# Kernel optimization log

Measured on AMD Instinct MI355X. Metric: run time of the kernel, lower is better.

Reference implementation:

```python
import jax, jax.numpy as jnp
import numpy as np

H, KV, Dh = 16, 4, 128
ROPE_BASE = 10000.0


def _rope(x, pos):
    # x: (B, nh, T, Dh); pos: (T,)
    inv = 1.0 / (ROPE_BASE ** (jnp.arange(0, Dh, 2, dtype=jnp.float32) / Dh))  # (Dh/2,)
    freqs = pos.astype(jnp.float32)[:, None] * inv[None, :]                    # (T, Dh/2)
    cos = jnp.cos(freqs).astype(x.dtype)[None, None]                           # (1,1,T,Dh/2)
    sin = jnp.sin(freqs).astype(x.dtype)[None, None]
    x1, x2 = x[..., ::2], x[..., 1::2]
    o1 = x1 * cos - x2 * sin
    o2 = x1 * sin + x2 * cos
    return jnp.stack([o1, o2], axis=-1).reshape(x.shape)


def setup_inputs() -> dict:
    key = jax.random.key(0)
    ks = jax.random.split(key, 5)
    B, T, d = 2, 2048, 2048
    s = 1.0 / np.sqrt(d)
    return {
        "x": jax.random.normal(ks[0], (B, T, d), dtype=jnp.float32),
        "Wq": jax.random.normal(ks[1], (d, H * Dh), dtype=jnp.float32) * s,
        "Wk": jax.random.normal(ks[2], (d, KV * Dh), dtype=jnp.float32) * s,
        "Wv": jax.random.normal(ks[3], (d, KV * Dh), dtype=jnp.float32) * s,
        "Wo": jax.random.normal(ks[4], (H * Dh, d), dtype=jnp.float32) * s,
    }


def reference(x, Wq, Wk, Wv, Wo):
    B, T, d = x.shape
    rep = H // KV
    q = (x @ Wq).reshape(B, T, H, Dh).transpose(0, 2, 1, 3)   # (B,H,T,Dh)
    k = (x @ Wk).reshape(B, T, KV, Dh).transpose(0, 2, 1, 3)  # (B,KV,T,Dh)
    v = (x @ Wv).reshape(B, T, KV, Dh).transpose(0, 2, 1, 3)

    pos = jnp.arange(T)
    q = _rope(q, pos)
    k = _rope(k, pos)

    # GQA repeat_kv: (B,KV,T,Dh) -> (B,H,T,Dh), heads repeated consecutively
    k_full = jnp.repeat(k, rep, axis=1)
    v_full = jnp.repeat(v, rep, axis=1)

    scale = 1.0 / np.sqrt(Dh)
    scores = jnp.einsum('bhqd,bhkd->bhqk', q, k_full) * scale  # (B,H,T,T)
    causal = jnp.tril(jnp.ones((T, T), dtype=bool))
    scores = jnp.where(causal[None, None], scores, -jnp.inf)
    attn = jax.nn.softmax(scores, axis=-1)
    out = jnp.einsum('bhqk,bhkd->bhqd', attn, v_full)          # (B,H,T,Dh)
    out = out.transpose(0, 2, 1, 3).reshape(B, T, H * Dh)
    return out @ Wo
```

## Files before the change

kernel.cpp:

```cpp
#include <hip/hip_runtime.h>
#include <stdint.h>

typedef __bf16 bf16;
typedef __bf16 bf16x8 __attribute__((ext_vector_type(8)));
typedef __bf16 bf16x4 __attribute__((ext_vector_type(4)));
typedef float  f32x4  __attribute__((ext_vector_type(4)));

#define T_SEQ  2048
#define NHEAD  16
#define DHEAD  128
#define DMODEL 2048
#define NQKV   3072
#define UNROLL _Pragma("unroll")

__device__ __forceinline__ void gload_lds16(const void* g, void* l) {
  __builtin_amdgcn_global_load_lds(
      (const __attribute__((address_space(1))) uint32_t*)g,
      (__attribute__((address_space(3))) uint32_t*)l, 16, 0, 0);
}

__device__ __forceinline__ void twt_body(const float* __restrict__ W,
                                         bf16* __restrict__ WT, int K, int N,
                                         int bx, int by, float (*t)[65]) {
  int k0 = bx * 64, n0 = by * 64;
  int r4 = threadIdx.x >> 6, c = threadIdx.x & 63;
#pragma unroll
  for (int i = 0; i < 16; i++) {
    int r = i * 4 + r4;
    t[r][c] = W[(size_t)(k0 + r) * N + n0 + c];
  }
  __syncthreads();
#pragma unroll
  for (int i = 0; i < 16; i++) {
    int r = i * 4 + r4;
    WT[(size_t)(n0 + r) * K + k0 + c] = (bf16)t[c][r];
  }
}

__global__ __launch_bounds__(256) void k_prep(const float* __restrict__ x,
                                              const float* __restrict__ Wq,
                                              const float* __restrict__ Wk,
                                              const float* __restrict__ Wv,
                                              const float* __restrict__ Wo,
                                              bf16* __restrict__ xb,
                                              bf16* __restrict__ WT,
                                              bf16* __restrict__ WoT) {
  __shared__ float t[64][65];
  const int blk = blockIdx.x;
  if (blk < 8192) {
    int i = (blk * 256 + threadIdx.x) * 4;
    float4 v = *(const float4*)(x + i);
    bf16x4 o = { (bf16)v.x, (bf16)v.y, (bf16)v.z, (bf16)v.w };
    *(bf16x4*)(xb + i) = o;
  } else if (blk < 9216) {
    int b = blk - 8192;
    twt_body(Wq, WT, 2048, 2048, b & 31, b >> 5, t);
  } else if (blk < 9472) {
    int b = blk - 9216;
    twt_body(Wk, WT + (size_t)2048 * 2048, 2048, 512, b & 31, b >> 5, t);
  } else if (blk < 9728) {
    int b = blk - 9472;
    twt_body(Wv, WT + (size_t)2560 * 2048, 2048, 512, b & 31, b >> 5, t);
  } else {
    int b = blk - 9728;
    twt_body(Wo, WoT, 2048, 2048, b & 31, b >> 5, t);
  }
}

__global__ __launch_bounds__(256) void k_post(bf16* __restrict__ QKV,
                                              bf16* __restrict__ Vtg) {
  __shared__ bf16 t[64][65];
  const int blk = blockIdx.x;
  if (blk < 5120) {
    const float L2B = 0.20762050593046007f;
    int tid = blk * 256 + threadIdx.x;
    int row = tid / 320;
    int c8 = (tid - row * 320) * 8;
    int tt = row & (T_SEQ - 1);
    bf16* p = QKV + (size_t)row * NQKV + c8;
    bf16x8 v = *(const bf16x8*)p;
    int ib = (c8 & 127) >> 1;
    bf16x8 o;
#pragma unroll
    for (int m = 0; m < 4; m++) {
      float inv = exp2f(-(float)(ib + m) * L2B);
      float ang = (float)tt * inv;
      float cs, sn;
      __sincosf(ang, &sn, &cs);
      float x1 = (float)v[2 * m], x2 = (float)v[2 * m + 1];
      o[2 * m]     = (bf16)(x1 * cs - x2 * sn);
      o[2 * m + 1] = (bf16)(x1 * sn + x2 * cs);
    }
    *(bf16x8*)p = o;
  } else {
    int bb = blk - 5120;
    int bx = bb & 31, by = (bb >> 5) & 1, g = bb >> 6;
    const int t0 = bx * 64, d0 = by * 64;
    const int b = g >> 2, kvh = g & 3;
    const bf16* src = QKV + (size_t)b * T_SEQ * NQKV + 2560 + kvh * DHEAD;
    bf16* dst = Vtg + ((size_t)(b * 4 + kvh) * 128 + d0) * T_SEQ + t0;
    const int r4 = threadIdx.x >> 6, c = threadIdx.x & 63;
#pragma unroll
    for (int i = 0; i < 16; i++) {
      int r = i * 4 + r4;
      t[r][c] = src[(size_t)(t0 + r) * NQKV + d0 + c];
    }
    __syncthreads();
#pragma unroll
    for (int i = 0; i < 16; i++) {
      int r = i * 4 + r4;
      dst[(size_t)r * T_SEQ + c] = t[c][r];
    }
  }
}

#define PH(BUF, P, RB, VMW, STAGE) do {                                                   \
    bf16x8 a0k0 = rdA(BUF, 2*(P),     0), a0k1 = rdA(BUF, 2*(P),     1);                  \
    bf16x8 a1k0 = rdA(BUF, 2*(P) + 1, 0), a1k1 = rdA(BUF, 2*(P) + 1, 1);                  \
    if (RB) {                                                                             \
      UNROLL for (int n = 0; n < 4; n++) { b0[n] = rdB(BUF, 0, n); b1[n] = rdB(BUF, 1, n); } \
    }                                                                                     \
    STAGE                                                                                 \
    __builtin_amdgcn_sched_barrier(0);                                                    \
    __builtin_amdgcn_s_barrier();                                                         \
    asm volatile("s_waitcnt lgkmcnt(0)" ::: "memory");                                    \
    __builtin_amdgcn_sched_barrier(0);                                                    \
    __builtin_amdgcn_s_setprio(1);                                                        \
    UNROLL for (int n = 0; n < 4; n++) {                                                  \
      acc[2*(P)][n]   = __builtin_amdgcn_mfma_f32_16x16x32_bf16(a0k0, b0[n], acc[2*(P)][n], 0, 0, 0);     \
      acc[2*(P)][n]   = __builtin_amdgcn_mfma_f32_16x16x32_bf16(a0k1, b1[n], acc[2*(P)][n], 0, 0, 0);     \
      acc[2*(P)+1][n] = __builtin_amdgcn_mfma_f32_16x16x32_bf16(a1k0, b0[n], acc[2*(P)+1][n], 0, 0, 0);   \
      acc[2*(P)+1][n] = __builtin_amdgcn_mfma_f32_16x16x32_bf16(a1k1, b1[n], acc[2*(P)+1][n], 0, 0, 0);   \
    }                                                                                     \
    __builtin_amdgcn_s_setprio(0);                                                        \
    if (VMW) { asm volatile("s_waitcnt vmcnt(4)" ::: "memory"); }                         \
    __builtin_amdgcn_sched_barrier(0);                                                    \
    __builtin_amdgcn_s_barrier();                                                         \
  } while (0)

template<bool F32OUT>
__global__ __launch_bounds__(512) void k_gemm2(const bf16* __restrict__ A,
                                               const bf16* __restrict__ BT,
                                               void* __restrict__ C,
                                               int M, int N, int K) {
  __shared__ __align__(16) bf16 L[2][2][2][8192];
  const int nwg = gridDim.x * gridDim.y;
  const int orig = blockIdx.y * gridDim.x + blockIdx.x;
  const int tile = (orig & 7) * (nwg >> 3) + (orig >> 3);
  const int m0 = (tile % gridDim.x) * 256, n0 = (tile / gridDim.x) * 256;
  const int tid = threadIdx.x;
  const int lane = tid & 63, w = tid >> 6;
  const int wr = w >> 2, wc = w & 3;
  const int l15 = lane & 15, lg = lane >> 4;
  const int srow = tid >> 3;
  const int scol = ((tid & 7) ^ (srow & 7)) * 8;
  const int NKT = K >> 6;

  f32x4 acc[8][4] = {};
  bf16x8 b0[4], b1[4];

  auto stA = [&](int buf, int half, int kt) {
    const bf16* g = A + (size_t)(m0 + half * 128 + srow) * K + kt * 64 + scol;
    bf16* lb = &L[buf][0][half][w * 512];
    gload_lds16(g, lb);
    gload_lds16(g + (size_t)64 * K, lb + 4096);
  };
  auto stB = [&](int buf, int half, int kt) {
    const bf16* g = BT + (size_t)(n0 + half * 128 + srow) * K + kt * 64 + scol;
    bf16* lb = &L[buf][1][half][w * 512];
    gload_lds16(g, lb);
    gload_lds16(g + (size_t)64 * K, lb + 4096);
  };
  auto rdA = [&](int buf, int fr, int kk) -> bf16x8 {
    int r = fr * 16 + l15;
    return *(const bf16x8*)((const char*)&L[buf][0][wr][0] + r * 128 +
                            (((kk * 4 + lg) ^ (r & 7)) << 4));
  };
  auto rdB = [&](int buf, int kk, int n) -> bf16x8 {
    int rr = wc * 64 + n * 16 + l15;
    return *(const bf16x8*)((const char*)&L[buf][1][rr >> 7][0] + (rr & 127) * 128 +
                            (((kk * 4 + lg) ^ (rr & 7)) << 4));
  };

  stA(0, 0, 0); stA(0, 1, 0);
  stB(0, 0, 0); stB(0, 1, 0);
  stB(1, 0, 1); stB(1, 1, 1);
  asm volatile("s_waitcnt vmcnt(4)" ::: "memory");
  __builtin_amdgcn_sched_barrier(0);
  __builtin_amdgcn_s_barrier();

  for (int it = 0; it < (NKT >> 1); ++it) {
    const int t1 = 2 * it + 1;
    const int t2 = (t1 + 1 < NKT) ? t1 + 1 : NKT - 1;
    const int t3 = (t1 + 2 < NKT) ? t1 + 2 : NKT - 1;
    PH(0, 0, 1, 0, stA(1, 0, t1););
    PH(0, 1, 0, 0, stA(1, 1, t1););
    PH(0, 2, 0, 0, stB(0, 0, t2););
    PH(0, 3, 0, 1, stB(0, 1, t2););
    PH(1, 0, 1, 0, stA(0, 0, t2););
    PH(1, 1, 0, 0, stA(0, 1, t2););
    PH(1, 2, 0, 0, stB(1, 0, t3););
    PH(1, 3, 0, 1, stB(1, 1, t3););
  }

  const int r0 = m0 + wr * 128 + lg * 4;
  const int c0 = n0 + wc * 64 + l15;
  UNROLL for (int m = 0; m < 8; m++)
    UNROLL for (int n = 0; n < 4; n++)
      UNROLL for (int i = 0; i < 4; i++) {
        size_t idx = (size_t)(r0 + m * 16 + i) * N + (c0 + n * 16);
        if (F32OUT) ((float*)C)[idx] = acc[m][n][i];
        else        ((bf16*)C)[idx]  = (bf16)acc[m][n][i];
      }
}

#define COMPUTE2(kt) do {                                                                 \
    f32x4 sA_[4] = {}, sB_[4] = {};                                                       \
    const char* ks_ = (const char*)Ks;                                                    \
    __builtin_amdgcn_s_setprio(1);                                                        \
    UNROLL for (int kk = 0; kk < 4; kk++)                                                 \
      UNROLL for (int n = 0; n < 4; n++) {                                                \
        int row_ = n * 16 + l15;                                                          \
        int cb_ = (kk * 64 + lg * 16) ^ ((row_ & 7) << 4);                                \
        bf16x8 kf_ = *(const bf16x8*)(ks_ + row_ * 256 + cb_);                            \
        sA_[n] = __builtin_amdgcn_mfma_f32_16x16x32_bf16(kf_, qA[kk], sA_[n], 0, 0, 0);   \
        sB_[n] = __builtin_amdgcn_mfma_f32_16x16x32_bf16(kf_, qB[kk], sB_[n], 0, 0, 0);   \
      }                                                                                   \
    __builtin_amdgcn_s_setprio(0);                                                        \
    __syncthreads();                               \
    if ((kt) + 1 < NT) issueK((kt) + 1);                \
    float vmA_ = -1e30f, vmB_ = -1e30f;                                                   \
    if ((kt) == qt) {                                                                     \
      UNROLL for (int n = 0; n < 4; n++)                                                  \
        UNROLL for (int i = 0; i < 4; i++) {                                              \
          if ((kt) * 64 + n * 16 + lg * 4 + i > qglob) {                                  \
            sA_[n][i] = -1e30f; sB_[n][i] = -1e30f;                                       \
          }                                                                               \
          vmA_ = fmaxf(vmA_, sA_[n][i]);                                                  \
          vmB_ = fmaxf(vmB_, sB_[n][i]);                                                  \
        }                                                                                 \
    } else {                                                                              \
      UNROLL for (int n = 0; n < 4; n++)                                                  \
        UNROLL for (int i = 0; i < 4; i++) {                                              \
          vmA_ = fmaxf(vmA_, sA_[n][i]);                                                  \
          vmB_ = fmaxf(vmB_, sB_[n][i]);                                                  \
        }                                                                                 \
    }                                                                                     \
    vmA_ = fmaxf(vmA_, __shfl_xor(vmA_, 16));                                             \
    vmA_ = fmaxf(vmA_, __shfl_xor(vmA_, 32));                                             \
    vmB_ = fmaxf(vmB_, __shfl_xor(vmB_, 16));                                             \
    vmB_ = fmaxf(vmB_, __shfl_xor(vmB_, 32));                                             \
    if (!__all((vmA_ <= mA + 8.0f) && (vmB_ <= mB + 8.0f))) {                             \
      float mnA_ = fmaxf(mA, vmA_), mnB_ = fmaxf(mB, vmB_);                               \
      float alA_ = __builtin_amdgcn_exp2f(mA - mnA_);                                     \
      float alB_ = __builtin_amdgcn_exp2f(mB - mnB_);                                     \
      mA = mnA_; mB = mnB_;                                                               \
      lA *= alA_; lB *= alB_;                                                             \
      UNROLL for (int i = 0; i < 4; i++) {                                                \
        int src_ = (lane & 48) + ((lane >> 2) & 12) + i;                                  \
        float aA_ = __shfl(alA_, src_);                                                   \
        float aB_ = __shfl(alB_, src_);                                                   \
        UNROLL for (int n = 0; n < 8; n++) { oA[n][i] *= aA_; oB[n][i] *= aB_; }          \
      }                                                                                   \
    }                                                                                     \
    bf16x8 paA0_, paA1_, paB0_, paB1_;                                                    \
    {                                                                                     \
      float rs_ = 0.f;                                                                    \
      UNROLL for (int n = 0; n < 4; n++) {                                                \
        bf16x4 pk_;                                                                       \
        UNROLL for (int i = 0; i < 4; i++) {                                              \
          float pv_ = __builtin_amdgcn_exp2f(sA_[n][i] - mA);                             \
          rs_ += pv_;                                                                     \
          pk_[i] = (bf16)pv_;                                                             \
        }                                                                                 \
        *(bf16x4*)(&Ps[w][l15][n * 16 + lg * 4]) = pk_;                                   \
      }                                                                                   \
      rs_ += __shfl_xor(rs_, 16);                                                         \
      rs_ += __shfl_xor(rs_, 32);                                                         \
      lA += rs_;                                                                          \
      paA0_ = *(const bf16x8*)(&Ps[w][l15][lg * 8]);                                      \
      paA1_ = *(const bf16x8*)(&Ps[w][l15][32 + lg * 8]);                                 \
    }                                                                                     \
    {                                                                                     \
      float rs_ = 0.f;                                                                    \
      UNROLL for (int n = 0; n < 4; n++) {                                                \
        bf16x4 pk_;                                                                       \
        UNROLL for (int i = 0; i < 4; i++) {                                              \
          float pv_ = __builtin_amdgcn_exp2f(sB_[n][i] - mB);                             \
          rs_ += pv_;                                                                     \
          pk_[i] = (bf16)pv_;                                                             \
        }                                                                                 \
        *(bf16x4*)(&Ps[w][l15][n * 16 + lg * 4]) = pk_;                                   \
      }                                                                                   \
      rs_ += __shfl_xor(rs_, 16);                                                         \
      rs_ += __shfl_xor(rs_, 32);                                                         \
      lB += rs_;                                                                          \
      paB0_ = *(const bf16x8*)(&Ps[w][l15][lg * 8]);                                      \
      paB1_ = *(const bf16x8*)(&Ps[w][l15][32 + lg * 8]);                                 \
    }                                                                                     \
    const char* vs_ = (const char*)Vs;                                                    \
    __builtin_amdgcn_s_setprio(1);                                                        \
    UNROLL for (int n = 0; n < 8; n++) {                                                  \
      int d_ = n * 16 + l15;                                                              \
      bf16x8 vf0_ = *(const bf16x8*)(vs_ + d_ * 128 + (((lg) ^ (d_ & 7)) << 4));          \
      oA[n] = __builtin_amdgcn_mfma_f32_16x16x32_bf16(paA0_, vf0_, oA[n], 0, 0, 0);       \
      oB[n] = __builtin_amdgcn_mfma_f32_16x16x32_bf16(paB0_, vf0_, oB[n], 0, 0, 0);       \
      bf16x8 vf1_ = *(const bf16x8*)(vs_ + d_ * 128 + (((4 + lg) ^ (d_ & 7)) << 4));      \
      oA[n] = __builtin_amdgcn_mfma_f32_16x16x32_bf16(paA1_, vf1_, oA[n], 0, 0, 0);       \
      oB[n] = __builtin_amdgcn_mfma_f32_16x16x32_bf16(paB1_, vf1_, oB[n], 0, 0, 0);       \
    }                                                                                     \
    __builtin_amdgcn_s_setprio(0);                                                        \
    __syncthreads();                             \
    if ((kt) + 1 < NT) issueV((kt) + 1);              \
  } while (0)

__global__ __launch_bounds__(256) void k_flash(const bf16* __restrict__ QKV,
                                               const bf16* __restrict__ Vtg,
                                               bf16* __restrict__ AO) {
  __shared__ __align__(16) bf16 Ks[64 * 128];
  __shared__ __align__(16) bf16 Vs[128 * 64];
  __shared__ __align__(16) bf16 Ps[4][16][72];
  const int orig = blockIdx.y * 32 + blockIdx.x;
  const int fin  = ((orig & 7) << 6) | (orig >> 3);
  const int bhp  = fin >> 5;
  const int qt   = 31 - (fin & 31);
  const int b = bhp >> 3, kvh = (bhp >> 1) & 3, hp = bhp & 1;
  const int h0 = kvh * 4 + hp * 2, h1 = h0 + 1;
  const int tid = threadIdx.x, lane = tid & 63, w = tid >> 6;
  const int l15 = lane & 15, lg = lane >> 4;
  const int qglob = qt * 64 + w * 16 + l15;
  const float qs = 0.12753102f;

  bf16x8 qA[4], qB[4];
  {
    const size_t qoA = (size_t)(b * T_SEQ + qt * 64 + w * 16 + l15) * NQKV + h0 * DHEAD;
    const size_t qoB = (size_t)(b * T_SEQ + qt * 64 + w * 16 + l15) * NQKV + h1 * DHEAD;
    UNROLL for (int kk = 0; kk < 4; kk++) {
      bf16x8 a = *(const bf16x8*)(QKV + qoA + kk * 32 + lg * 8);
      bf16x8 bb = *(const bf16x8*)(QKV + qoB + kk * 32 + lg * 8);
      UNROLL for (int j = 0; j < 8; j++) {
        a[j] = (bf16)((float)a[j] * qs);
        bb[j] = (bf16)((float)bb[j] * qs);
      }
      qA[kk] = a; qB[kk] = bb;
    }
  }

  f32x4 oA[8] = {}, oB[8] = {};
  float mA = -1e30f, mB = -1e30f, lA = 0.f, lB = 0.f;

  const bf16* Kbase = QKV + (size_t)b * T_SEQ * NQKV + DMODEL + kvh * DHEAD;
  const bf16* Vbase = Vtg + (size_t)(b * 4 + kvh) * 128 * T_SEQ;

  auto issueK = [&](int kt) {
    UNROLL for (int i = 0; i < 4; i++) {
      int row = w * 16 + i * 4 + lg;
      int col = (l15 ^ (row & 7)) * 8;
      gload_lds16(Kbase + (size_t)(kt * 64 + row) * NQKV + col,
                  Ks + (w * 4 + i) * 512);
    }
  };
  auto issueV = [&](int kt) {
    UNROLL for (int i = 0; i < 4; i++) {
      int d = (w * 4 + i) * 8 + (lane >> 3);
      int u = lane & 7;
      gload_lds16(Vbase + (size_t)d * T_SEQ + kt * 64 + ((u ^ (d & 7)) * 8),
                  Vs + (w * 4 + i) * 512);
    }
  };

  issueK(0);
  issueV(0);
  __syncthreads();

  const int NT = qt + 1;
  for (int kt = 0; kt < NT; kt++) {
    COMPUTE2(kt);
  }

  {
    const size_t ob0 = (size_t)(b * T_SEQ + qt * 64 + w * 16 + lg * 4) * DMODEL + h0 * DHEAD + l15;
    const size_t ob1 = (size_t)(b * T_SEQ + qt * 64 + w * 16 + lg * 4) * DMODEL + h1 * DHEAD + l15;
    UNROLL for (int i = 0; i < 4; i++) {
      int src = (lane & 48) + ((lane >> 2) & 12) + i;
      float invA = 1.0f / __shfl(lA, src);
      float invB = 1.0f / __shfl(lB, src);
      UNROLL for (int n = 0; n < 8; n++) {
        AO[ob0 + (size_t)i * DMODEL + n * 16] = (bf16)(oA[n][i] * invA);
        AO[ob1 + (size_t)i * DMODEL + n * 16] = (bf16)(oB[n][i] * invB);
      }
    }
  }
}

extern "C" void kernel_launch(void* const* d_in, const int* in_sizes, int n_in,
                              void* d_out, int out_size, void* d_ws, size_t ws_size,
                              hipStream_t stream) {
  const float* x  = (const float*)d_in[0];
  const float* Wq = (const float*)d_in[1];
  const float* Wk = (const float*)d_in[2];
  const float* Wv = (const float*)d_in[3];
  const float* Wo = (const float*)d_in[4];
  char* ws = (char*)d_ws;
  bf16* xb  = (bf16*)ws;
  bf16* WT  = (bf16*)(ws + 16777216ull);
  bf16* WoT = (bf16*)(ws + 16777216ull + 12582912ull);
  bf16* QKV = (bf16*)(ws + 16777216ull + 12582912ull + 8388608ull);
  bf16* AO  = (bf16*)(ws + 16777216ull + 12582912ull + 8388608ull + 25165824ull);
  bf16* Vtg = WT;
  float* out = (float*)d_out;

  k_prep<<<10752, 256, 0, stream>>>(x, Wq, Wk, Wv, Wo, xb, WT, WoT);
  k_gemm2<false><<<dim3(16, 12), 512, 0, stream>>>(xb, WT, QKV, 4096, 3072, 2048);
  k_post<<<5632, 256, 0, stream>>>(QKV, Vtg);
  k_flash<<<dim3(32, 16), 256, 0, stream>>>(QKV, Vtg, AO);
  k_gemm2<true><<<dim3(16, 8), 512, 0, stream>>>(AO, WoT, out, 4096, 2048, 2048);
}
```

Baseline: 205.7 us.

## Use 256x128-tile GEMM for output projection and rebalance flash tile mapping

Adds a new GEMM kernel with 256x128 tiles (each wave computes 128x32) for the output projection, doubling the grid to 256 workgroups so more CUs are busy on the MI355X. It keeps LDS double buffering with phased barriers and waits. It also remaps flash-attention blocks so each XCD gets a head pair, with the first half of the launch taking short causal tiles and the second half long ones. This is meant to improve load balance and L2 locality. The smaller N tile lowers reuse of A per workgroup, which raises the A traffic.

```diff
diff --git a/kernel.cpp b/kernel.cpp
--- a/kernel.cpp
+++ b/kernel.cpp
@@ -212,6 +212,101 @@
         if (F32OUT) ((float*)C)[idx] = acc[m][n][i];
         else        ((bf16*)C)[idx]  = (bf16)acc[m][n][i];
       }
+}
+
+#define PH2(BUF, P, RB, VMW, STAGE) do {                                                  \
+    bf16x8 a0k0 = rdA(BUF, 2*(P),     0), a0k1 = rdA(BUF, 2*(P),     1);                  \
+    bf16x8 a1k0 = rdA(BUF, 2*(P) + 1, 0), a1k1 = rdA(BUF, 2*(P) + 1, 1);                  \
+    if (RB) {                                                                             \
+      UNROLL for (int n = 0; n < 2; n++) { b0[n] = rdB(BUF, 0, n); b1[n] = rdB(BUF, 1, n); } \
+    }                                                                                     \
+    STAGE                                                                                 \
+    __builtin_amdgcn_sched_barrier(0);                                                    \
+    __builtin_amdgcn_s_barrier();                                                         \
+    asm volatile("s_waitcnt lgkmcnt(0)" ::: "memory");                                    \
+    __builtin_amdgcn_sched_barrier(0);                                                    \
+    __builtin_amdgcn_s_setprio(1);                                                        \
+    UNROLL for (int n = 0; n < 2; n++) {                                                  \
+      acc[2*(P)][n]   = __builtin_amdgcn_mfma_f32_16x16x32_bf16(a0k0, b0[n], acc[2*(P)][n], 0, 0, 0);     \
+      acc[2*(P)][n]   = __builtin_amdgcn_mfma_f32_16x16x32_bf16(a0k1, b1[n], acc[2*(P)][n], 0, 0, 0);     \
+      acc[2*(P)+1][n] = __builtin_amdgcn_mfma_f32_16x16x32_bf16(a1k0, b0[n], acc[2*(P)+1][n], 0, 0, 0);   \
+      acc[2*(P)+1][n] = __builtin_amdgcn_mfma_f32_16x16x32_bf16(a1k1, b1[n], acc[2*(P)+1][n], 0, 0, 0);   \
+    }                                                                                     \
+    __builtin_amdgcn_s_setprio(0);                                                        \
+    if (VMW) { asm volatile("s_waitcnt vmcnt(2)" ::: "memory"); }                         \
+    __builtin_amdgcn_sched_barrier(0);                                                    \
+    __builtin_amdgcn_s_barrier();                                                         \
+  } while (0)
+
+__global__ __launch_bounds__(512) void k_gemm3(const bf16* __restrict__ A,
+                                               const bf16* __restrict__ BT,
+                                               float* __restrict__ C,
+                                               int M, int N, int K) {
+  __shared__ __align__(16) bf16 L[2][3][8192];
+  const int nwg = gridDim.x * gridDim.y;
+  const int orig = blockIdx.y * gridDim.x + blockIdx.x;
+  const int tile = (orig & 7) * (nwg >> 3) + (orig >> 3);
+  const int m0 = (tile % gridDim.x) * 256, n0 = (tile / gridDim.x) * 128;
+  const int tid = threadIdx.x;
+  const int lane = tid & 63, w = tid >> 6;
+  const int wr = w >> 2, wc = w & 3;
+  const int l15 = lane & 15, lg = lane >> 4;
+  const int srow = tid >> 3;
+  const int scol = ((tid & 7) ^ (srow & 7)) * 8;
+  const int NKT = K >> 6;
+
+  f32x4 acc[8][2] = {};
+  bf16x8 b0[2], b1[2];
+
+  auto stA = [&](int buf, int half, int kt) {
+    const bf16* g = A + (size_t)(m0 + half * 128 + srow) * K + kt * 64 + scol;
+    bf16* lb = &L[buf][half][w * 512];
+    gload_lds16(g, lb);
+    gload_lds16(g + (size_t)64 * K, lb + 4096);
+  };
+  auto stB = [&](int buf, int kt) {
+    const bf16* g = BT + (size_t)(n0 + srow) * K + kt * 64 + scol;
+    bf16* lb = &L[buf][2][w * 512];
+    gload_lds16(g, lb);
+    gload_lds16(g + (size_t)64 * K, lb + 4096);
+  };
+  auto rdA = [&](int buf, int fr, int kk) -> bf16x8 {
+    int r = fr * 16 + l15;
+    return *(const bf16x8*)((const char*)&L[buf][wr][0] + r * 128 +
+                            (((kk * 4 + lg) ^ (r & 7)) << 4));
+  };
+  auto rdB = [&](int buf, int kk, int n) -> bf16x8 {
+    int rr = wc * 32 + n * 16 + l15;
+    return *(const bf16x8*)((const char*)&L[buf][2][0] + rr * 128 +
+                            (((kk * 4 + lg) ^ (rr & 7)) << 4));
+  };
+
+  stA(0, 0, 0); stA(0, 1, 0); stB(0, 0);
+  stB(1, 1);
+  asm volatile("s_waitcnt vmcnt(2)" ::: "memory");
+  __builtin_amdgcn_sched_barrier(0);
+  __builtin_amdgcn_s_barrier();
+
+  for (int it = 0; it < (NKT >> 1); ++it) {
+    const int t1 = 2 * it + 1;
+    const int t2 = (t1 + 1 < NKT) ? t1 + 1 : NKT - 1;
+    const int t3 = (t1 + 2 < NKT) ? t1 + 2 : NKT - 1;
+    PH2(0, 0, 1, 0, stA(1, 0, t1););
+    PH2(0, 1, 0, 0, stA(1, 1, t1););
+    PH2(0, 2, 0, 0, stB(0, t2););
+    PH2(0, 3, 0, 1, ;);
+    PH2(1, 0, 1, 0, stA(0, 0, t2););
+    PH2(1, 1, 0, 0, stA(0, 1, t2););
+    PH2(1, 2, 0, 0, stB(1, t3););
+    PH2(1, 3, 0, 1, ;);
+  }
+
+  const int r0 = m0 + wr * 128 + lg * 4;
+  const int c0 = n0 + wc * 32 + l15;
+  UNROLL for (int m = 0; m < 8; m++)
+    UNROLL for (int n = 0; n < 2; n++)
+      UNROLL for (int i = 0; i < 4; i++)
+        C[(size_t)(r0 + m * 16 + i) * N + (c0 + n * 16)] = acc[m][n][i];
 }
 
 #define COMPUTE2(kt) do {                                                                 \
@@ -321,9 +416,10 @@
   __shared__ __align__(16) bf16 Vs[128 * 64];
   __shared__ __align__(16) bf16 Ps[4][16][72];
   const int orig = blockIdx.y * 32 + blockIdx.x;
-  const int fin  = ((orig & 7) << 6) | (orig >> 3);
-  const int bhp  = fin >> 5;
-  const int qt   = 31 - (fin & 31);
+  const int z = orig >> 8, c = orig & 255;
+  const int xcd = c & 7, u = c >> 3;
+  const int bhp = (xcd << 1) | (u >> 4);
+  const int qt  = z ? (31 - (u & 15)) : (u & 15);
   const int b = bhp >> 3, kvh = (bhp >> 1) & 3, hp = bhp & 1;
   const int h0 = kvh * 4 + hp * 2, h1 = h0 + 1;
   const int tid = threadIdx.x, lane = tid & 63, w = tid >> 6;
@@ -363,8 +459,8 @@
   auto issueV = [&](int kt) {
     UNROLL for (int i = 0; i < 4; i++) {
       int d = (w * 4 + i) * 8 + (lane >> 3);
-      int u = lane & 7;
-      gload_lds16(Vbase + (size_t)d * T_SEQ + kt * 64 + ((u ^ (d & 7)) * 8),
+      int u2 = lane & 7;
+      gload_lds16(Vbase + (size_t)d * T_SEQ + kt * 64 + ((u2 ^ (d & 7)) * 8),
                   Vs + (w * 4 + i) * 512);
     }
   };
@@ -414,5 +510,5 @@
   k_gemm2<false><<<dim3(16, 12), 512, 0, stream>>>(xb, WT, QKV, 4096, 3072, 2048);
   k_post<<<5632, 256, 0, stream>>>(QKV, Vtg);
   k_flash<<<dim3(32, 16), 256, 0, stream>>>(QKV, Vtg, AO);
-  k_gemm2<true><<<dim3(16, 8), 512, 0, stream>>>(AO, WoT, out, 4096, 2048, 2048);
-}
+  k_gemm3<<<dim3(16, 16), 512, 0, stream>>>(AO, WoT, out, 4096, 2048, 2048);
+}
```

Result: no change. 207.6 us (+0.9%).
